# Performance work log

Measured on AMD Instinct MI355X. Metric: run time of the kernel, lower is better.

The kernel has to match this reference:

```python
import jax, jax.numpy as jnp
import numpy as np

IN_C, OUT_C, K, STRIDE, PAD = 64, 128, 3, 1, 1
GRID_SIZE, SPLINE_ORDER = 5, 3
GRID_LO, GRID_HI = -1.0, 1.0
IN_DIM = IN_C * K * K  # groups=1 -> 576


def setup_inputs() -> dict:
    key = jax.random.key(0)
    k0, k1, k2, k3 = jax.random.split(key, 4)
    x = jax.random.normal(k0, (16, IN_C, 48, 48), dtype=jnp.float32)
    base_weight = jax.random.normal(k1, (OUT_C, IN_DIM), dtype=jnp.float32) * 0.05
    spline_weight = jax.random.normal(k2, (OUT_C, IN_DIM, GRID_SIZE + SPLINE_ORDER), dtype=jnp.float32) * 0.05
    spline_scaler = 1.0 + jax.random.normal(k3, (OUT_C, IN_DIM), dtype=jnp.float32) * 0.05
    return {"x": x, "base_weight": base_weight, "spline_weight": spline_weight, "spline_scaler": spline_scaler}


def _grid():
    # uniform extended grid, shape (IN_DIM, GRID_SIZE + 2*SPLINE_ORDER + 1)
    h = (GRID_HI - GRID_LO) / GRID_SIZE
    g = jnp.arange(-SPLINE_ORDER, GRID_SIZE + SPLINE_ORDER + 1, dtype=jnp.float32) * h + GRID_LO
    return jnp.broadcast_to(g, (IN_DIM, g.shape[0]))


def b_splines(x, grid):
    # x: (N, in_dim); grid: (in_dim, G). Cox-de Boor recursion.
    xe = x[..., None]
    bases = ((xe >= grid[:, :-1]) & (xe < grid[:, 1:])).astype(x.dtype)
    for k in range(1, SPLINE_ORDER + 1):
        left = (xe - grid[:, : -(k + 1)]) / (grid[:, k:-1] - grid[:, : -(k + 1)]) * bases[..., :-1]
        right = (grid[:, k + 1:] - xe) / (grid[:, k + 1:] - grid[:, 1:-k]) * bases[..., 1:]
        bases = left + right
    return bases  # (N, in_dim, GRID_SIZE + SPLINE_ORDER)


def reference(x, base_weight, spline_weight, spline_scaler):
    B, C, H, W = x.shape
    # im2col: feature dim ordered (c, kh, kw) with spatial fastest, matching F.unfold
    patches = jax.lax.conv_general_dilated_patches(
        x, (K, K), (STRIDE, STRIDE), [(PAD, PAD), (PAD, PAD)],
        dimension_numbers=("NCHW", "OIHW", "NCHW"))  # (B, IN_DIM, Ho, Wo)
    Ho = (H + 2 * PAD - (K - 1) - 1) // STRIDE + 1
    Wo = (W + 2 * PAD - (K - 1) - 1) // STRIDE + 1
    # faithful to the source: view(B, groups, in_dim, L) then view(-1, in_dim), no transpose
    x_unf = patches.reshape(B, 1, IN_DIM, Ho * Wo).reshape(-1, IN_DIM)  # (B*L, IN_DIM)
    grid = _grid()
    base = jax.nn.silu(x_unf) @ base_weight.T  # (N, OUT_C)
    scaled_sw = spline_weight * spline_scaler[..., None]  # (OUT_C, IN_DIM, Gc)
    spl = b_splines(x_unf, grid).reshape(x_unf.shape[0], -1) @ scaled_sw.reshape(OUT_C, -1).T
    return (base + spl).reshape(B, OUT_C, Ho, Wo)
```

## Files before the change

### kernel.cpp

```cpp
#include <hip/hip_runtime.h>
#include <hip/hip_bf16.h>

#define B_N    16
#define C_IN   64
#define QDIM   576
#define OC     128
#define M_TOT  36864
#define NKT    81
#define PLANE  2512

typedef __attribute__((ext_vector_type(8))) short short8;
typedef __attribute__((ext_vector_type(4))) float floatx4;

__device__ __forceinline__ unsigned short f2bf(float f) {
    union { float f; unsigned u; } v; v.f = f;
    unsigned r = (v.u + 0x7FFFu + ((v.u >> 16) & 1u)) >> 16;
    return (unsigned short)r;
}

__device__ __forceinline__ void compute_phi(float x, float* phi) {
    phi[0] = x * __builtin_amdgcn_rcpf(1.0f + __expf(-x));
    float t[12];
#pragma unroll
    for (int i = 0; i < 12; ++i) t[i] = 0.4f * (float)(i - 3) - 1.0f;
    float bb[11];
#pragma unroll
    for (int j = 0; j < 11; ++j) bb[j] = (x >= t[j] && x < t[j + 1]) ? 1.0f : 0.0f;
#pragma unroll
    for (int j = 0; j < 10; ++j)
        bb[j] = (x - t[j]) * 2.5f * bb[j] + (t[j + 2] - x) * 2.5f * bb[j + 1];
#pragma unroll
    for (int j = 0; j < 9; ++j)
        bb[j] = (x - t[j]) * 1.25f * bb[j] + (t[j + 3] - x) * 1.25f * bb[j + 1];
#pragma unroll
    for (int j = 0; j < 8; ++j)
        bb[j] = (x - t[j]) * (2.5f / 3.0f) * bb[j] + (t[j + 4] - x) * (2.5f / 3.0f) * bb[j + 1];
#pragma unroll
    for (int g = 0; g < 8; ++g) phi[1 + g] = bb[g];
}

__global__ __launch_bounds__(256) void phi_kernel(const float* __restrict__ x,
                                                  unsigned short* __restrict__ Phi) {
    int ch = blockIdx.x * 256 + threadIdx.x;
    int bc = ch / 314;
    int cp = ch - bc * 314;
    int p0 = cp * 8;
    const float* xsrc = x + (size_t)bc * 2304;
    short8 v[9];
#pragma unroll
    for (int e = 0; e < 8; ++e) {
        int p = p0 + e;
        int hh = p / 50;
        int ww = p - hh * 50;
        float xv = (hh >= 1 && hh <= 48 && ww >= 1 && ww <= 48) ? xsrc[(hh - 1) * 48 + (ww - 1)] : 0.0f;
        float phi[9];
        compute_phi(xv, phi);
#pragma unroll
        for (int j = 0; j < 9; ++j) v[j][e] = (short)f2bf(phi[j]);
    }
    unsigned short* pdst = Phi + (size_t)bc * 9 * PLANE + p0;
#pragma unroll
    for (int j = 0; j < 9; ++j) *(short8*)(pdst + (size_t)j * PLANE) = v[j];
}

__global__ __launch_bounds__(256) void pack_kernel(const float* __restrict__ bw,
                                                   const float* __restrict__ sw,
                                                   const float* __restrict__ sc,
                                                   unsigned short* __restrict__ Wp) {
    int gtid = blockIdx.x * 256 + threadIdx.x;
    int oc = gtid / QDIM, q = gtid % QDIM;
    float base = bw[gtid];
    float scal = sc[gtid];
    unsigned char* wp8 = (unsigned char*)Wp;
    int off_oq = (oc * 128 + (q & 63) * 2) ^ ((oc & 7) << 4);
    int ktb = q >> 6;
    *(unsigned short*)(wp8 + (size_t)ktb * 16384 + off_oq) = f2bf(base);
#pragma unroll
    for (int g = 0; g < 8; ++g) {
        float v = sw[(size_t)gtid * 8 + g] * scal;
        *(unsigned short*)(wp8 + (size_t)((g + 1) * 9 + ktb) * 16384 + off_oq) = f2bf(v);
    }
}

__global__ __launch_bounds__(256, 3) void gemm_kernel(const unsigned short* __restrict__ Phi,
                                                      const unsigned short* __restrict__ Wp,
                                                      float* __restrict__ out) {
    __shared__ __align__(16) unsigned char lds[45056];
    int bid = blockIdx.x;
    int swzb = (bid & 7) * 96 + (bid >> 3);
    int m0 = swzb * 48;
    int tid = threadIdx.x;
    int lane = tid & 63;
    int wv = tid >> 6;
    int wo = wv & 1, wk = wv >> 1;
    int lo = lane & 15, hi = lane >> 4, l7 = lane & 7;

    int s8 = tid & 7;
    int rA = tid >> 3;
    int sxA = s8 ^ (rA & 7);
    int rB = (tid < 128) ? (32 + (tid >> 3)) : rA;
    int sxB = s8 ^ (rB & 7);

    size_t rowb[2];
    int rows[2] = {rA, rB};
#pragma unroll
    for (int i = 0; i < 2; ++i) {
        int n  = m0 + rows[i];
        int b  = n / 2304;
        int u  = n - b * 2304;
        int du = u >> 2;
        int r  = u & 3;
        int c  = du / 9;
        int tap = du - c * 9;
        int kh = tap / 3, kw = tap - kh * 3;
        rowb[i] = ((size_t)(b * C_IN + c) * 9) * PLANE + (size_t)((r * 12 + kh) * 50 + kw);
    }

    auto stage = [&](int sel, int kt) {
        int j  = kt / 9;
        int q0 = (kt - j * 9) << 6;
        unsigned char* pb = lds + 32768 + sel * 6144;
        {
            int qs = q0 + sxA * 8;
            int hq = qs / 48, wq = qs - hq * 48;
            const unsigned short* src = Phi + rowb[0] + (size_t)j * PLANE + (size_t)(hq * 50 + wq);
            __builtin_amdgcn_global_load_lds((const __attribute__((address_space(1))) void*)src,
                                             (__attribute__((address_space(3))) void*)(pb + tid * 16), 16, 0, 0);
        }
        if (tid < 128) {
            int qs = q0 + sxB * 8;
            int hq = qs / 48, wq = qs - hq * 48;
            const unsigned short* src = Phi + rowb[1] + (size_t)j * PLANE + (size_t)(hq * 50 + wq);
            __builtin_amdgcn_global_load_lds((const __attribute__((address_space(1))) void*)src,
                                             (__attribute__((address_space(3))) void*)(pb + 4096 + tid * 16), 16, 0, 0);
        }
        const unsigned char* ws = (const unsigned char*)Wp + (size_t)kt * 16384;
        unsigned char* wb = lds + sel * 16384;
#pragma unroll
        for (int i = 0; i < 4; ++i)
            __builtin_amdgcn_global_load_lds((const __attribute__((address_space(1))) void*)(ws + i * 4096 + tid * 16),
                                             (__attribute__((address_space(3))) void*)(wb + i * 4096 + tid * 16), 16, 0, 0);
    };

    floatx4 acc[3][4];
    floatx4 zz = {0.f, 0.f, 0.f, 0.f};
#pragma unroll
    for (int a = 0; a < 3; ++a)
#pragma unroll
        for (int b = 0; b < 4; ++b) acc[a][b] = zz;

    int sxr = ((wk * 4 + hi) ^ l7) << 4;
    int arow[3], brow[4];
#pragma unroll
    for (int fm = 0; fm < 3; ++fm) arow[fm] = (fm * 16 + lo) * 128;
#pragma unroll
    for (int fo = 0; fo < 4; ++fo) brow[fo] = (wo * 64 + fo * 16 + lo) * 128;

    auto compute = [&](int sel) {
        const unsigned char* wb = lds + sel * 16384;
        const unsigned char* pb = lds + 32768 + sel * 6144;
        short8 af[3], bf[4];
#pragma unroll
        for (int fm = 0; fm < 3; ++fm) af[fm] = *(const short8*)(pb + arow[fm] + sxr);
#pragma unroll
        for (int fo = 0; fo < 4; ++fo) bf[fo] = *(const short8*)(wb + brow[fo] + sxr);
#pragma unroll
        for (int fm = 0; fm < 3; ++fm)
#pragma unroll
            for (int fo = 0; fo < 4; ++fo)
                acc[fm][fo] = __builtin_amdgcn_mfma_f32_16x16x32_bf16(af[fm], bf[fo], acc[fm][fo], 0, 0, 0);
    };

    stage(0, 0);
    __syncthreads();
#pragma unroll 2
    for (int kt = 0; kt < NKT; ++kt) {
        if (kt + 1 < NKT) stage((kt + 1) & 1, kt + 1);
        compute(kt & 1);
        __syncthreads();
    }

    float* red = (float*)lds;
    if (wk == 1) {
#pragma unroll
        for (int fm = 0; fm < 3; ++fm)
#pragma unroll
            for (int fo = 0; fo < 4; ++fo)
#pragma unroll
                for (int r = 0; r < 4; ++r)
                    red[(wo * 48 + fm * 16 + hi * 4 + r) * 65 + fo * 16 + lo] = acc[fm][fo][r];
    }
    __syncthreads();
    if (wk == 0) {
#pragma unroll
        for (int fm = 0; fm < 3; ++fm) {
#pragma unroll
            for (int fo = 0; fo < 4; ++fo) {
                int oc = wo * 64 + fo * 16 + lo;
#pragma unroll
                for (int r = 0; r < 4; ++r) {
                    int nrow = m0 + fm * 16 + hi * 4 + r;
                    out[(size_t)nrow * 128 + oc] =
                        acc[fm][fo][r] + red[(wo * 48 + fm * 16 + hi * 4 + r) * 65 + fo * 16 + lo];
                }
            }
        }
    }
}

extern "C" void kernel_launch(void* const* d_in, const int* in_sizes, int n_in,
                              void* d_out, int out_size, void* d_ws, size_t ws_size,
                              hipStream_t stream) {
    const float* x  = (const float*)d_in[0];
    const float* bw = (const float*)d_in[1];
    const float* sw = (const float*)d_in[2];
    const float* sc = (const float*)d_in[3];
    float* out = (float*)d_out;

    unsigned short* Wp  = (unsigned short*)d_ws;
    unsigned short* Phi = (unsigned short*)((char*)d_ws + 1572864);

    pack_kernel<<<288, 256, 0, stream>>>(bw, sw, sc, Wp);
    phi_kernel<<<1256, 256, 0, stream>>>(x, Phi);
    gemm_kernel<<<M_TOT / 48, 256, 0, stream>>>(Phi, Wp, out);
}
```

Baseline: 149.6 us.

## Load GEMM weight fragments straight into registers, bypassing LDS

Weights are repacked in the pack kernel so each MFMA B-fragment sits contiguously for a lane. The GEMM then reads those fragments from global memory directly into registers, double-buffered one K-tile ahead, and only the Phi tiles are still staged through LDS. This removes the LDS writes and reads for weights and shrinks shared memory enough to allow four blocks per CU instead of three. The cost is more VGPRs for the two weight buffers and global-load latency that is hidden by only one tile of prefetch.

```diff
diff --git a/kernel.cpp b/kernel.cpp
--- a/kernel.cpp
+++ b/kernel.cpp
@@ -72,20 +72,22 @@
     float base = bw[gtid];
     float scal = sc[gtid];
     unsigned char* wp8 = (unsigned char*)Wp;
-    int off_oq = (oc * 128 + (q & 63) * 2) ^ ((oc & 7) << 4);
+    int kk = q & 63;
+    int inner = (oc >> 4) * 2048 + (kk >> 5) * 1024
+              + ((((kk >> 3) & 3) << 4) + (oc & 15)) * 16 + (kk & 7) * 2;
     int ktb = q >> 6;
-    *(unsigned short*)(wp8 + (size_t)ktb * 16384 + off_oq) = f2bf(base);
+    *(unsigned short*)(wp8 + (size_t)ktb * 16384 + inner) = f2bf(base);
 #pragma unroll
     for (int g = 0; g < 8; ++g) {
         float v = sw[(size_t)gtid * 8 + g] * scal;
-        *(unsigned short*)(wp8 + (size_t)((g + 1) * 9 + ktb) * 16384 + off_oq) = f2bf(v);
-    }
-}
-
-__global__ __launch_bounds__(256, 3) void gemm_kernel(const unsigned short* __restrict__ Phi,
+        *(unsigned short*)(wp8 + (size_t)((g + 1) * 9 + ktb) * 16384 + inner) = f2bf(v);
+    }
+}
+
+__global__ __launch_bounds__(256, 4) void gemm_kernel(const unsigned short* __restrict__ Phi,
                                                       const unsigned short* __restrict__ Wp,
                                                       float* __restrict__ out) {
-    __shared__ __align__(16) unsigned char lds[45056];
+    __shared__ __align__(16) unsigned char lds[24960];
     int bid = blockIdx.x;
     int swzb = (bid & 7) * 96 + (bid >> 3);
     int m0 = swzb * 48;
@@ -116,10 +118,10 @@
         rowb[i] = ((size_t)(b * C_IN + c) * 9) * PLANE + (size_t)((r * 12 + kh) * 50 + kw);
     }
 
-    auto stage = [&](int sel, int kt) {
+    auto stageA = [&](int sel, int kt) {
         int j  = kt / 9;
         int q0 = (kt - j * 9) << 6;
-        unsigned char* pb = lds + 32768 + sel * 6144;
+        unsigned char* pb = lds + sel * 6144;
         {
             int qs = q0 + sxA * 8;
             int hq = qs / 48, wq = qs - hq * 48;
@@ -134,12 +136,14 @@
             __builtin_amdgcn_global_load_lds((const __attribute__((address_space(1))) void*)src,
                                              (__attribute__((address_space(3))) void*)(pb + 4096 + tid * 16), 16, 0, 0);
         }
-        const unsigned char* ws = (const unsigned char*)Wp + (size_t)kt * 16384;
-        unsigned char* wb = lds + sel * 16384;
-#pragma unroll
-        for (int i = 0; i < 4; ++i)
-            __builtin_amdgcn_global_load_lds((const __attribute__((address_space(1))) void*)(ws + i * 4096 + tid * 16),
-                                             (__attribute__((address_space(3))) void*)(wb + i * 4096 + tid * 16), 16, 0, 0);
+    };
+
+    const unsigned char* wsrc = (const unsigned char*)Wp
+                              + (size_t)(wo * 4) * 2048 + (size_t)wk * 1024 + (size_t)lane * 16;
+    auto loadW = [&](short8* wf, int kt) {
+        const unsigned char* s = wsrc + (size_t)kt * 16384;
+#pragma unroll
+        for (int fo = 0; fo < 4; ++fo) wf[fo] = *(const short8*)(s + fo * 2048);
     };
 
     floatx4 acc[3][4];
@@ -150,33 +154,33 @@
         for (int b = 0; b < 4; ++b) acc[a][b] = zz;
 
     int sxr = ((wk * 4 + hi) ^ l7) << 4;
-    int arow[3], brow[4];
+    int arow[3];
 #pragma unroll
     for (int fm = 0; fm < 3; ++fm) arow[fm] = (fm * 16 + lo) * 128;
-#pragma unroll
-    for (int fo = 0; fo < 4; ++fo) brow[fo] = (wo * 64 + fo * 16 + lo) * 128;
-
-    auto compute = [&](int sel) {
-        const unsigned char* wb = lds + sel * 16384;
-        const unsigned char* pb = lds + 32768 + sel * 6144;
-        short8 af[3], bf[4];
+
+    auto compute = [&](int sel, const short8* wf) {
+        const unsigned char* pb = lds + sel * 6144;
+        short8 af[3];
 #pragma unroll
         for (int fm = 0; fm < 3; ++fm) af[fm] = *(const short8*)(pb + arow[fm] + sxr);
 #pragma unroll
-        for (int fo = 0; fo < 4; ++fo) bf[fo] = *(const short8*)(wb + brow[fo] + sxr);
-#pragma unroll
         for (int fm = 0; fm < 3; ++fm)
 #pragma unroll
             for (int fo = 0; fo < 4; ++fo)
-                acc[fm][fo] = __builtin_amdgcn_mfma_f32_16x16x32_bf16(af[fm], bf[fo], acc[fm][fo], 0, 0, 0);
+                acc[fm][fo] = __builtin_amdgcn_mfma_f32_16x16x32_bf16(af[fm], wf[fo], acc[fm][fo], 0, 0, 0);
     };
 
-    stage(0, 0);
+    short8 wA[4], wB[4];
+    stageA(0, 0);
+    loadW(wA, 0);
     __syncthreads();
-#pragma unroll 2
-    for (int kt = 0; kt < NKT; ++kt) {
-        if (kt + 1 < NKT) stage((kt + 1) & 1, kt + 1);
-        compute(kt & 1);
+    for (int kt = 0; kt < NKT; kt += 2) {
+        if (kt + 1 < NKT) { stageA(1, kt + 1); loadW(wB, kt + 1); }
+        compute(0, wA);
+        __syncthreads();
+        if (kt + 1 >= NKT) break;
+        if (kt + 2 < NKT) { stageA(0, kt + 2); loadW(wA, kt + 2); }
+        compute(1, wB);
         __syncthreads();
     }
 
```

Result: slower. 246.5 us (+64.7%).
